# Performance work log

Measured on AMD Instinct MI355X. Metric: run time of the kernel, lower is better.

## Reference

```python
import jax, jax.numpy as jnp
import numpy as np

B = 64      # 'batch' init arg: projected-away input dim
N = 8192    # sequence length after transpose
DK = 64     # dk, used only for 1/sqrt(dk) scaling


def setup_inputs() -> dict:
    key = jax.random.key(0)
    ks = jax.random.split(key, 9)
    f32 = jnp.float32
    q = jax.random.normal(ks[0], (B, N), f32)
    k = jax.random.normal(ks[1], (B, N), f32)
    v = jax.random.normal(ks[2], (B, N), f32)
    # Linear(B -> 1) params, torch-style: weight [1, B], bias [1]
    s = 1.0 / np.sqrt(B)
    Wq = jax.random.uniform(ks[3], (1, B), f32, -s, s)
    bq = jax.random.uniform(ks[4], (1,), f32, -s, s)
    Wk = jax.random.uniform(ks[5], (1, B), f32, -s, s)
    bk = jax.random.uniform(ks[6], (1,), f32, -s, s)
    Wv = jax.random.uniform(ks[7], (1, B), f32, -s, s)
    bv = jax.random.uniform(ks[8], (1,), f32, -s, s)
    return {"q": q, "k": k, "v": v, "Wq": Wq, "bq": bq,
            "Wk": Wk, "bk": bk, "Wv": Wv, "bv": bv}


def reference(q, k, v, Wq, bq, Wk, bk, Wv, bv):
    # q,k,v: [B, N]; transpose(0,1) then Linear(B -> 1) => [N, 1]
    qp = q.T @ Wq.T + bq          # [N, 1]
    kp = k.T @ Wk.T + bk          # [N, 1]
    vp = v.T @ Wv.T + bv          # [N, 1]
    scale = 1.0 / jnp.sqrt(jnp.asarray(DK, q.dtype))
    scores = (qp @ kp.T) * scale  # [N, N] rank-1 outer product
    attn = jax.nn.softmax(scores, axis=-1)  # [N, N]
    out = attn @ vp               # [N, 1]
    return (out, attn)
```

## Files before the change

### kernel.cpp

```cpp
#include <hip/hip_runtime.h>

#define N 8192
#define LOG2E 1.4426950408889634f
#define LN2   0.6931471805599453f
#define NMOM  15

using f4 = __attribute__((ext_vector_type(4))) float;

#if __has_builtin(__builtin_amdgcn_exp2f)
#define EXP2(x) __builtin_amdgcn_exp2f(x)
#else
#define EXP2(x) exp2f(x)
#endif

__global__ __launch_bounds__(256) void proj_kernel(
    const float* __restrict__ q, const float* __restrict__ k, const float* __restrict__ v,
    const float* __restrict__ Wq, const float* __restrict__ bq,
    const float* __restrict__ Wk, const float* __restrict__ bk,
    const float* __restrict__ Wv, const float* __restrict__ bv,
    float* __restrict__ aq, float* __restrict__ kp, float* __restrict__ pmom)
{
    const int tn = threadIdx.x & 63;
    const int tb = threadIdx.x >> 6;
    const int n  = blockIdx.x * 64 + tn;
    float sq = 0.f, sk = 0.f, sv = 0.f;
#pragma unroll
    for (int bi = 0; bi < 16; ++bi) {
        const int b = tb * 16 + bi;
        sq = fmaf(q[b * N + n], Wq[b], sq);
        sk = fmaf(k[b * N + n], Wk[b], sk);
        sv = fmaf(v[b * N + n], Wv[b], sv);
    }
    __shared__ float red[3][4][64];
    red[0][tb][tn] = sq; red[1][tb][tn] = sk; red[2][tb][tn] = sv;
    __syncthreads();
    if (tb == 0) {
        const float fq = red[0][0][tn] + red[0][1][tn] + red[0][2][tn] + red[0][3][tn];
        const float fk = red[1][0][tn] + red[1][1][tn] + red[1][2][tn] + red[1][3][tn];
        const float fv = red[2][0][tn] + red[2][1][tn] + red[2][2][tn] + red[2][3][tn];
        aq[n] = (fq + bq[0]) * 0.125f * LOG2E;
        const float kq = fk + bk[0];
        const float vq = fv + bv[0];
        kp[n] = kq;

        float pm[NMOM], pt[NMOM];
        float p = 1.f;
#pragma unroll
        for (int j = 0; j < NMOM; ++j) { pm[j] = p; pt[j] = vq * p; p *= kq; }
#pragma unroll
        for (int off = 32; off; off >>= 1) {
#pragma unroll
            for (int j = 0; j < NMOM; ++j) {
                pm[j] += __shfl_xor(pm[j], off);
                pt[j] += __shfl_xor(pt[j], off);
            }
        }
        if (tn == 0) {
            float* pb = pmom + blockIdx.x * 32;
#pragma unroll
            for (int j = 0; j < NMOM; ++j) { pb[j] = pm[j]; pb[16 + j] = pt[j]; }
            pb[15] = 0.f; pb[31] = 0.f;
        }
    }
}

__global__ __launch_bounds__(256, 4) void attn_kernel(
    const float* __restrict__ aq, const float* __restrict__ kp,
    const float* __restrict__ pmom,
    float* __restrict__ out, float* __restrict__ attn)
{
    __shared__ float kl[N];
    __shared__ float psum[32][8];
    __shared__ float mm[32];
    __shared__ float rowA[8], rowC[8];
    const int tid = threadIdx.x, lane = tid & 63, wave = tid >> 6;

    f4 stg[8];
#pragma unroll
    for (int it = 0; it < 8; ++it)
        stg[it] = reinterpret_cast<const f4*>(kp)[tid + it * 256];

    {
        const int j = tid >> 3, c = tid & 7;
        float s = 0.f;
#pragma unroll
        for (int i = 0; i < 16; ++i)
            s += pmom[(c * 16 + i) * 32 + j];
        psum[j][c] = s;
    }
#pragma unroll
    for (int it = 0; it < 8; ++it)
        reinterpret_cast<f4*>(kl)[tid + it * 256] = stg[it];
    __syncthreads();
    if (tid < 32) {
        float s = 0.f;
#pragma unroll
        for (int c = 0; c < 8; ++c) s += psum[tid][c];
        mm[tid] = s;
    }
    __syncthreads();
    if (tid < 8) {
        static const float invf[NMOM] = {
            1.0f, 1.0f, 0.5f, 1.6666666666666666e-01f, 4.1666666666666664e-02f,
            8.3333333333333332e-03f, 1.3888888888888889e-03f, 1.9841269841269841e-04f,
            2.4801587301587302e-05f, 2.7557319223985893e-06f, 2.7557319223985888e-07f,
            2.5052108385441720e-08f, 2.0876756987868100e-09f, 1.6059043836821613e-10f,
            1.1470745597729725e-11f };
        const int r = blockIdx.x * 8 + tid;
        const float a2 = aq[r];
        const float b  = a2 * LN2;
        float s = mm[NMOM - 1] * invf[NMOM - 1];
        float t = mm[16 + NMOM - 1] * invf[NMOM - 1];
#pragma unroll
        for (int nn = NMOM - 2; nn >= 0; --nn) {
            s = fmaf(s, b, mm[nn] * invf[nn]);
            t = fmaf(t, b, mm[16 + nn] * invf[nn]);
        }
        out[r] = t / s;
        rowA[tid] = a2;
        rowC[tid] = -__log2f(s);
    }
    __syncthreads();

#pragma unroll 1
    for (int rr = 0; rr < 2; ++rr) {
        const int ri = wave * 2 + rr;
        const int r  = blockIdx.x * 8 + ri;
        const float a = rowA[ri];
        const float c = rowC[ri];
        f4* __restrict__ arow = reinterpret_cast<f4*>(attn + (size_t)r * N);
#pragma unroll 8
        for (int it = 0; it < 32; ++it) {
            const f4 kk = reinterpret_cast<const f4*>(kl)[lane + it * 64];
            f4 w;
            w[0] = EXP2(fmaf(a, kk[0], c));
            w[1] = EXP2(fmaf(a, kk[1], c));
            w[2] = EXP2(fmaf(a, kk[2], c));
            w[3] = EXP2(fmaf(a, kk[3], c));
            arow[lane + it * 64] = w;
        }
    }
}

extern "C" void kernel_launch(void* const* d_in, const int* in_sizes, int n_in,
                              void* d_out, int out_size, void* d_ws, size_t ws_size,
                              hipStream_t stream)
{
    const float* q  = (const float*)d_in[0];
    const float* k  = (const float*)d_in[1];
    const float* v  = (const float*)d_in[2];
    const float* Wq = (const float*)d_in[3];
    const float* bq = (const float*)d_in[4];
    const float* Wk = (const float*)d_in[5];
    const float* bk = (const float*)d_in[6];
    const float* Wv = (const float*)d_in[7];
    const float* bv = (const float*)d_in[8];

    float* out  = (float*)d_out;
    float* attn = out + N;

    float* aq   = (float*)d_ws;
    float* kp   = aq + N;
    float* pmom = kp + N;

    proj_kernel<<<128, 256, 0, stream>>>(q, k, v, Wq, bq, Wk, bk, Wv, bv, aq, kp, pmom);
    attn_kernel<<<1024, 256, 0, stream>>>(aq, kp, pmom, out, attn);
}
```

Before: 53.27 us.

## Split per-row constants into separate kernel and stream k directly from global

```diff
diff --git a/kernel.cpp b/kernel.cpp
--- a/kernel.cpp
+++ b/kernel.cpp
@@ -64,81 +64,73 @@
     }
 }
 
-__global__ __launch_bounds__(256, 4) void attn_kernel(
-    const float* __restrict__ aq, const float* __restrict__ kp,
-    const float* __restrict__ pmom,
-    float* __restrict__ out, float* __restrict__ attn)
+__global__ __launch_bounds__(512) void const_kernel(
+    const float* __restrict__ aq, const float* __restrict__ pmom,
+    float* __restrict__ out, float* __restrict__ cc)
 {
-    __shared__ float kl[N];
-    __shared__ float psum[32][8];
-    __shared__ float mm[32];
-    __shared__ float rowA[8], rowC[8];
-    const int tid = threadIdx.x, lane = tid & 63, wave = tid >> 6;
-
-    f4 stg[8];
-#pragma unroll
-    for (int it = 0; it < 8; ++it)
-        stg[it] = reinterpret_cast<const f4*>(kp)[tid + it * 256];
-
+    __shared__ float psum[32][16];
+    __shared__ float M[32];
+    const int tid = threadIdx.x;
     {
-        const int j = tid >> 3, c = tid & 7;
+        const int j = tid >> 4;
+        const int c = tid & 15;
         float s = 0.f;
 #pragma unroll
-        for (int i = 0; i < 16; ++i)
-            s += pmom[(c * 16 + i) * 32 + j];
+        for (int i = 0; i < 8; ++i) s += pmom[(c * 8 + i) * 32 + j];
         psum[j][c] = s;
     }
-#pragma unroll
-    for (int it = 0; it < 8; ++it)
-        reinterpret_cast<f4*>(kl)[tid + it * 256] = stg[it];
     __syncthreads();
     if (tid < 32) {
-        float s = 0.f;
-#pragma unroll
-        for (int c = 0; c < 8; ++c) s += psum[tid][c];
-        mm[tid] = s;
-    }
-    __syncthreads();
-    if (tid < 8) {
-        static const float invf[NMOM] = {
+        static const float invf16[16] = {
             1.0f, 1.0f, 0.5f, 1.6666666666666666e-01f, 4.1666666666666664e-02f,
             8.3333333333333332e-03f, 1.3888888888888889e-03f, 1.9841269841269841e-04f,
             2.4801587301587302e-05f, 2.7557319223985893e-06f, 2.7557319223985888e-07f,
             2.5052108385441720e-08f, 2.0876756987868100e-09f, 1.6059043836821613e-10f,
-            1.1470745597729725e-11f };
-        const int r = blockIdx.x * 8 + tid;
-        const float a2 = aq[r];
-        const float b  = a2 * LN2;
-        float s = mm[NMOM - 1] * invf[NMOM - 1];
-        float t = mm[16 + NMOM - 1] * invf[NMOM - 1];
+            1.1470745597729725e-11f, 0.0f };
+        float s = 0.f;
 #pragma unroll
-        for (int nn = NMOM - 2; nn >= 0; --nn) {
-            s = fmaf(s, b, mm[nn] * invf[nn]);
-            t = fmaf(t, b, mm[16 + nn] * invf[nn]);
-        }
-        out[r] = t / s;
-        rowA[tid] = a2;
-        rowC[tid] = -__log2f(s);
+        for (int c = 0; c < 16; ++c) s += psum[tid][c];
+        M[tid] = s * invf16[tid & 15];
     }
     __syncthreads();
+    const int r = blockIdx.x * 512 + tid;
+    const float a2 = aq[r];
+    const float b  = a2 * LN2;
+    float s = M[NMOM - 1], t = M[16 + NMOM - 1];
+#pragma unroll
+    for (int nn = NMOM - 2; nn >= 0; --nn) {
+        s = fmaf(s, b, M[nn]);
+        t = fmaf(t, b, M[16 + nn]);
+    }
+    out[r] = t / s;
+    cc[r] = -__log2f(s);
+}
 
-#pragma unroll 1
-    for (int rr = 0; rr < 2; ++rr) {
-        const int ri = wave * 2 + rr;
-        const int r  = blockIdx.x * 8 + ri;
-        const float a = rowA[ri];
-        const float c = rowC[ri];
-        f4* __restrict__ arow = reinterpret_cast<f4*>(attn + (size_t)r * N);
+__global__ __launch_bounds__(256) void attn_kernel(
+    const float* __restrict__ kp, const float* __restrict__ aq,
+    const float* __restrict__ cc, float* __restrict__ attn)
+{
+    const int tid = threadIdx.x, lane = tid & 63, wave = tid >> 6;
+    const int r0 = blockIdx.x * 8 + wave * 2;
+    const float a0 = aq[r0],     c0 = cc[r0];
+    const float a1 = aq[r0 + 1], c1 = cc[r0 + 1];
+    const f4* __restrict__ kp4 = reinterpret_cast<const f4*>(kp);
+    f4* __restrict__ arow0 = reinterpret_cast<f4*>(attn + (size_t)r0 * N);
+    f4* __restrict__ arow1 = reinterpret_cast<f4*>(attn + (size_t)(r0 + 1) * N);
 #pragma unroll 8
-        for (int it = 0; it < 32; ++it) {
-            const f4 kk = reinterpret_cast<const f4*>(kl)[lane + it * 64];
-            f4 w;
-            w[0] = EXP2(fmaf(a, kk[0], c));
-            w[1] = EXP2(fmaf(a, kk[1], c));
-            w[2] = EXP2(fmaf(a, kk[2], c));
-            w[3] = EXP2(fmaf(a, kk[3], c));
-            arow[lane + it * 64] = w;
-        }
+    for (int it = 0; it < 32; ++it) {
+        const f4 kk = kp4[lane + it * 64];
+        f4 w0, w1;
+        w0[0] = EXP2(fmaf(a0, kk[0], c0));
+        w0[1] = EXP2(fmaf(a0, kk[1], c0));
+        w0[2] = EXP2(fmaf(a0, kk[2], c0));
+        w0[3] = EXP2(fmaf(a0, kk[3], c0));
+        w1[0] = EXP2(fmaf(a1, kk[0], c1));
+        w1[1] = EXP2(fmaf(a1, kk[1], c1));
+        w1[2] = EXP2(fmaf(a1, kk[2], c1));
+        w1[3] = EXP2(fmaf(a1, kk[3], c1));
+        arow0[lane + it * 64] = w0;
+        arow1[lane + it * 64] = w1;
     }
 }
 
@@ -159,10 +151,12 @@
     float* out  = (float*)d_out;
     float* attn = out + N;
 
-    float* aq   = (float*)d_ws;
-    float* kp   = aq + N;
-    float* pmom = kp + N;
+    float* kp   = (float*)d_ws;
+    float* aq   = kp + N;
+    float* cc   = aq + N;
+    float* pmom = cc + N;
 
     proj_kernel<<<128, 256, 0, stream>>>(q, k, v, Wq, bq, Wk, bk, Wv, bv, aq, kp, pmom);
-    attn_kernel<<<1024, 256, 0, stream>>>(aq, kp, pmom, out, attn);
+    const_kernel<<<16, 512, 0, stream>>>(aq, pmom, out, cc);
+    attn_kernel<<<1024, 256, 0, stream>>>(kp, aq, cc, attn);
 }
```

Result: slower. 54.57 us (+2.4%).

## Drop LDS staging of keys, read kp from cache, one row per wave

Applied to the files above, without the earlier changes.

```diff
diff --git a/kernel.cpp b/kernel.cpp
--- a/kernel.cpp
+++ b/kernel.cpp
@@ -64,57 +64,46 @@
     }
 }
 
-__global__ __launch_bounds__(256, 4) void attn_kernel(
+__global__ __launch_bounds__(256, 8) void attn_kernel(
     const float* __restrict__ aq, const float* __restrict__ kp,
     const float* __restrict__ pmom,
     float* __restrict__ out, float* __restrict__ attn)
 {
-    __shared__ float kl[N];
     __shared__ float psum[32][8];
-    __shared__ float mm[32];
-    __shared__ float rowA[8], rowC[8];
+    __shared__ float M[32];
+    __shared__ float rowA[4], rowC[4];
     const int tid = threadIdx.x, lane = tid & 63, wave = tid >> 6;
-
-    f4 stg[8];
-#pragma unroll
-    for (int it = 0; it < 8; ++it)
-        stg[it] = reinterpret_cast<const f4*>(kp)[tid + it * 256];
 
     {
         const int j = tid >> 3, c = tid & 7;
         float s = 0.f;
 #pragma unroll
-        for (int i = 0; i < 16; ++i)
-            s += pmom[(c * 16 + i) * 32 + j];
+        for (int i = 0; i < 16; ++i) s += pmom[(c * 16 + i) * 32 + j];
         psum[j][c] = s;
     }
-#pragma unroll
-    for (int it = 0; it < 8; ++it)
-        reinterpret_cast<f4*>(kl)[tid + it * 256] = stg[it];
     __syncthreads();
     if (tid < 32) {
-        float s = 0.f;
-#pragma unroll
-        for (int c = 0; c < 8; ++c) s += psum[tid][c];
-        mm[tid] = s;
-    }
-    __syncthreads();
-    if (tid < 8) {
-        static const float invf[NMOM] = {
+        static const float invf16[16] = {
             1.0f, 1.0f, 0.5f, 1.6666666666666666e-01f, 4.1666666666666664e-02f,
             8.3333333333333332e-03f, 1.3888888888888889e-03f, 1.9841269841269841e-04f,
             2.4801587301587302e-05f, 2.7557319223985893e-06f, 2.7557319223985888e-07f,
             2.5052108385441720e-08f, 2.0876756987868100e-09f, 1.6059043836821613e-10f,
-            1.1470745597729725e-11f };
-        const int r = blockIdx.x * 8 + tid;
+            1.1470745597729725e-11f, 0.0f };
+        float s = 0.f;
+#pragma unroll
+        for (int c = 0; c < 8; ++c) s += psum[tid][c];
+        M[tid] = s * invf16[tid & 15];
+    }
+    __syncthreads();
+    if (tid < 4) {
+        const int r = blockIdx.x * 4 + tid;
         const float a2 = aq[r];
         const float b  = a2 * LN2;
-        float s = mm[NMOM - 1] * invf[NMOM - 1];
-        float t = mm[16 + NMOM - 1] * invf[NMOM - 1];
+        float s = M[NMOM - 1], t = M[16 + NMOM - 1];
 #pragma unroll
         for (int nn = NMOM - 2; nn >= 0; --nn) {
-            s = fmaf(s, b, mm[nn] * invf[nn]);
-            t = fmaf(t, b, mm[16 + nn] * invf[nn]);
+            s = fmaf(s, b, M[nn]);
+            t = fmaf(t, b, M[16 + nn]);
         }
         out[r] = t / s;
         rowA[tid] = a2;
@@ -122,23 +111,20 @@
     }
     __syncthreads();
 
-#pragma unroll 1
-    for (int rr = 0; rr < 2; ++rr) {
-        const int ri = wave * 2 + rr;
-        const int r  = blockIdx.x * 8 + ri;
-        const float a = rowA[ri];
-        const float c = rowC[ri];
-        f4* __restrict__ arow = reinterpret_cast<f4*>(attn + (size_t)r * N);
-#pragma unroll 8
-        for (int it = 0; it < 32; ++it) {
-            const f4 kk = reinterpret_cast<const f4*>(kl)[lane + it * 64];
-            f4 w;
-            w[0] = EXP2(fmaf(a, kk[0], c));
-            w[1] = EXP2(fmaf(a, kk[1], c));
-            w[2] = EXP2(fmaf(a, kk[2], c));
-            w[3] = EXP2(fmaf(a, kk[3], c));
-            arow[lane + it * 64] = w;
-        }
+    const int r = blockIdx.x * 4 + wave;
+    const float a = rowA[wave];
+    const float c = rowC[wave];
+    const f4* __restrict__ kp4 = reinterpret_cast<const f4*>(kp);
+    f4* __restrict__ arow = reinterpret_cast<f4*>(attn + (size_t)r * N);
+#pragma unroll 4
+    for (int it = 0; it < 32; ++it) {
+        const f4 kk = kp4[lane + it * 64];
+        f4 w;
+        w[0] = EXP2(fmaf(a, kk[0], c));
+        w[1] = EXP2(fmaf(a, kk[1], c));
+        w[2] = EXP2(fmaf(a, kk[2], c));
+        w[3] = EXP2(fmaf(a, kk[3], c));
+        arow[lane + it * 64] = w;
     }
 }
 
@@ -159,10 +145,10 @@
     float* out  = (float*)d_out;
     float* attn = out + N;
 
-    float* aq   = (float*)d_ws;
-    float* kp   = aq + N;
-    float* pmom = kp + N;
+    float* kp   = (float*)d_ws;
+    float* aq   = kp + N;
+    float* pmom = aq + N;
 
     proj_kernel<<<128, 256, 0, stream>>>(q, k, v, Wq, bq, Wk, bk, Wv, bv, aq, kp, pmom);
-    attn_kernel<<<1024, 256, 0, stream>>>(aq, kp, pmom, out, attn);
+    attn_kernel<<<2048, 256, 0, stream>>>(aq, kp, pmom, out, attn);
 }
```

New measurement: 55.46 us. +4.1%, slower.
